# Kernel tuning notes

Hardware: AMD Instinct MI355X
Metric: run time of the kernel (lower is better)

The kernel has to match this reference:

```python
import jax, jax.numpy as jnp
import numpy as np

MAXG = 8          # max adaptive sampling grid (boxes generated so ceil(roi_size) <= 8)
SCALE = 0.125     # spatial_scale / ds (ds = 1.0)


def setup_inputs() -> dict:
    key = jax.random.key(0)
    ks = jax.random.split(key, 12)
    bs, N, ch, H, W = 8, 128, 1280, 64, 64
    out_ch, inner = 1024, 5120
    z = jax.random.normal(ks[0], (bs, ch, H, W), jnp.float32)
    # boxes (x1, y1, x2, y2) in 512x512 image coords, sizes in [8, 64] px
    x1 = jax.random.uniform(ks[1], (bs, N), minval=0.0, maxval=448.0)
    y1 = jax.random.uniform(ks[2], (bs, N), minval=0.0, maxval=448.0)
    bw = jax.random.uniform(ks[3], (bs, N), minval=8.0, maxval=64.0)
    bh = jax.random.uniform(ks[4], (bs, N), minval=8.0, maxval=64.0)
    bboxes = jnp.stack([x1, y1, x1 + bw, y1 + bh], axis=-1)

    def lin(k, fan_in, shape):
        return jax.random.normal(k, shape, jnp.float32) * (1.0 / np.sqrt(fan_in))

    W1 = lin(ks[5], ch, (ch, inner)); b1 = jnp.zeros((inner,), jnp.float32)
    W2 = lin(ks[6], inner, (inner, out_ch)); b2 = jnp.zeros((out_ch,), jnp.float32)
    S1 = lin(ks[7], 2, (2, 64)); sb1 = jnp.zeros((64,), jnp.float32)
    S2 = lin(ks[8], 64, (64, 256)); sb2 = jnp.zeros((256,), jnp.float32)
    S3 = lin(ks[9], 256, (256, out_ch)); sb3 = jnp.zeros((out_ch,), jnp.float32)
    O = lin(ks[10], 2 * out_ch, (2 * out_ch, out_ch)); ob = jnp.zeros((out_ch,), jnp.float32)
    return dict(z=z, bboxes=bboxes, W1=W1, b1=b1, W2=W2, b2=b2,
                S1=S1, sb1=sb1, S2=S2, sb2=sb2, S3=S3, sb3=sb3, O=O, ob=ob)


def _prep(c, size):
    # torchvision bilinear border handling for one coordinate axis
    oob = (c < -1.0) | (c > size)
    cc = jnp.clip(c, 0.0, None)
    lo0 = jnp.floor(cc)
    hi_case = lo0 >= size - 1
    lo = jnp.minimum(lo0, size - 1).astype(jnp.int32)
    hi = jnp.minimum(lo0 + 1, size - 1).astype(jnp.int32)
    frac = jnp.where(hi_case, 0.0, cc - lo0)
    return lo, hi, frac, oob


def _roi_align_1x1(z, bboxes):
    # torchvision roi_align, output_size=1, aligned=True, sampling_ratio=-1
    bs, ch, H, W = z.shape
    N = bboxes.shape[1]
    boxes = jax.lax.stop_gradient(bboxes).reshape(-1, 4) * SCALE - 0.5  # aligned
    bidx = jnp.repeat(jnp.arange(bs), N)
    rw = boxes[:, 2] - boxes[:, 0]
    rh = boxes[:, 3] - boxes[:, 1]
    gw = jnp.clip(jnp.ceil(rw), 1, MAXG)   # adaptive grid: ceil(roi_size / 1)
    gh = jnp.clip(jnp.ceil(rh), 1, MAXG)
    count = gh * gw
    i = jnp.arange(MAXG, dtype=jnp.float32)
    ys = boxes[:, 1:2] + (i[None] + 0.5) * rh[:, None] / gh[:, None]  # [R, G]
    xs = boxes[:, 0:1] + (i[None] + 0.5) * rw[:, None] / gw[:, None]
    vy = i[None] < gh[:, None]
    vx = i[None] < gw[:, None]
    yl, yh, fy, oy = _prep(ys, H)
    xl, xh, fx, ox = _prep(xs, W)
    my = (vy & ~oy).astype(z.dtype)
    mx = (vx & ~ox).astype(z.dtype)
    mask = my[:, :, None] * mx[:, None, :]             # [R, G, G]
    hy, ly = 1.0 - fy, fy
    hx, lx = 1.0 - fx, fx
    zt = jnp.transpose(z, (0, 2, 3, 1))                # [bs, H, W, ch]
    acc = jnp.zeros((bs * N, ch), z.dtype)
    corners = [(yl, xl, hy, hx), (yl, xh, hy, lx), (yh, xl, ly, hx), (yh, xh, ly, lx)]
    for yi, xi, wy, wx in corners:
        wt = mask * (wy[:, :, None] * wx[:, None, :])  # [R, G, G]
        v = zt[bidx[:, None, None], yi[:, :, None], xi[:, None, :]]  # [R, G, G, ch]
        acc = acc + jnp.einsum('rgh,rghc->rc', wt, v)
    return (acc / count[:, None]).reshape(bs, N, ch)


def reference(z, bboxes, W1, b1, W2, b2, S1, sb1, S2, sb2, S3, sb3, O, ob):
    x = _roi_align_1x1(z, bboxes)                      # [bs, N, ch]
    x = jax.nn.relu(x @ W1 + b1) @ W2 + b2             # out MLP
    # BBoxSizeEmbedder: (h, w) = (y2 - y1, x2 - x1)
    sz = jnp.stack([bboxes[..., 3] - bboxes[..., 1],
                    bboxes[..., 2] - bboxes[..., 0]], axis=-1)
    e = jax.nn.relu(sz @ S1 + sb1)
    e = jax.nn.relu(e @ S2 + sb2)
    e = e @ S3 + sb3
    return jnp.concatenate([x, e], axis=-1) @ O + ob   # out2
```

## Files before the change

kernel.cpp:

```cpp
#include <hip/hip_runtime.h>

static constexpr int kBS    = 8;
static constexpr int kNROI  = 128;
static constexpr int kR     = kBS * kNROI;
static constexpr int kCH    = 1280;
static constexpr int kH     = 64;
static constexpr int kW     = 64;
static constexpr int kPIX   = kH * kW;
static constexpr int kINNER = 5120;
static constexpr int kOUTC  = 1024;
static constexpr int kXE    = 2 * kOUTC;
static constexpr int kE2    = 256;
static constexpr int kLB    = 144;

typedef _Float16 half8 __attribute__((ext_vector_type(8)));
typedef float floatx4 __attribute__((ext_vector_type(4)));

__device__ __forceinline__ void gload_lds16(const _Float16* g, _Float16* l) {
    __builtin_amdgcn_global_load_lds(
        (const __attribute__((address_space(1))) void*)g,
        (__attribute__((address_space(3))) void*)l,
        16, 0, 0);
}

static constexpr int kPrepListEnd = 4;
static constexpr int kPrepMlpEnd  = 260;
static constexpr int kPrepAllEnd  = 260 + 13824;

__global__ __launch_bounds__(256) void prep_all(const float* __restrict__ W1,
                                                const float* __restrict__ W2,
                                                const float* __restrict__ O,
                                                const float* __restrict__ S3,
                                                _Float16* __restrict__ W1t,
                                                _Float16* __restrict__ W2t,
                                                _Float16* __restrict__ Ot,
                                                _Float16* __restrict__ S3t,
                                                const float* __restrict__ bboxes,
                                                const float* __restrict__ S1,
                                                const float* __restrict__ sb1,
                                                const float* __restrict__ S2,
                                                const float* __restrict__ sb2,
                                                _Float16* __restrict__ h2f,
                                                int2* __restrict__ lst,
                                                int* __restrict__ npA) {
    __shared__ float smem[12 * 256 * 2];
    const int bid = blockIdx.x;
    const int t   = threadIdx.x;

    if (bid < kPrepListEnd) {
        float* yw = smem;
        float* xw = smem + 12 * 256;
        const int r = bid * 256 + t;
#pragma unroll
        for (int i = 0; i < 12; ++i) { yw[i * 256 + t] = 0.0f; xw[i * 256 + t] = 0.0f; }

        const float x1 = bboxes[r * 4 + 0] * 0.125f - 0.5f;
        const float y1 = bboxes[r * 4 + 1] * 0.125f - 0.5f;
        const float x2 = bboxes[r * 4 + 2] * 0.125f - 0.5f;
        const float y2 = bboxes[r * 4 + 3] * 0.125f - 0.5f;
        const float rw = x2 - x1, rh = y2 - y1;
        const float gwf = fminf(fmaxf(ceilf(rw), 1.0f), 8.0f);
        const float ghf = fminf(fmaxf(ceilf(rh), 1.0f), 8.0f);
        const int gw = (int)gwf, gh = (int)ghf;
        const float ic = 1.0f / (gwf * ghf);

        int ymin = 0, last = 0;
        for (int g = 0; g < gh; ++g) {
            const float c   = y1 + ((float)g + 0.5f) * rh / ghf;
            const bool oob  = (c < -1.0f) || (c > 64.0f);
            const float cc  = fmaxf(c, 0.0f);
            const float lo0 = floorf(cc);
            const bool hic  = (lo0 >= 63.0f);
            const int lo    = (int)fminf(lo0, 63.0f);
            const int hi    = (int)fminf(lo0 + 1.0f, 63.0f);
            const float fr  = hic ? 0.0f : (cc - lo0);
            const float m   = oob ? 0.0f : 1.0f;
            if (g == 0) ymin = lo;
            const int il = min(lo - ymin, 11);
            const int ih = min(hi - ymin, 11);
            yw[il * 256 + t] += m * (1.0f - fr);
            yw[ih * 256 + t] += m * fr;
            last = hi;
        }
        const int nyd = min(last - ymin + 1, 12);

        int xmin = 0; last = 0;
        for (int g = 0; g < gw; ++g) {
            const float c   = x1 + ((float)g + 0.5f) * rw / gwf;
            const bool oob  = (c < -1.0f) || (c > 64.0f);
            const float cc  = fmaxf(c, 0.0f);
            const float lo0 = floorf(cc);
            const bool hic  = (lo0 >= 63.0f);
            const int lo    = (int)fminf(lo0, 63.0f);
            const int hi    = (int)fminf(lo0 + 1.0f, 63.0f);
            const float fr  = hic ? 0.0f : (cc - lo0);
            const float m   = oob ? 0.0f : 1.0f;
            if (g == 0) xmin = lo;
            const int il = min(lo - xmin, 11);
            const int ih = min(hi - xmin, 11);
            xw[il * 256 + t] += m * (1.0f - fr);
            xw[ih * 256 + t] += m * fr;
            last = hi;
        }
        const int nxd = min(last - xmin + 1, 12);

        int2* lr = lst + (size_t)r * kLB;
        int p = 0;
        for (int iy = 0; iy < nyd; ++iy) {
            const float wy = yw[iy * 256 + t] * ic;
            const int yb   = (ymin + iy) * kW + xmin;
            for (int ix = 0; ix < nxd; ++ix) {
                const float w = wy * xw[ix * 256 + t];
                if (w != 0.0f) {
                    int2 e; e.x = yb + ix; e.y = __float_as_int(w);
                    lr[p++] = e;
                }
            }
        }
        npA[r] = p;
    } else if (bid < kPrepMlpEnd) {
        const int r0 = (bid - kPrepListEnd) * 4;
        float* sz = smem;
        float* h1 = smem + 8;
        if (t < 8) {
            const int row = t >> 1;
            const int c   = t & 1;
            const float* bb = bboxes + (size_t)(r0 + row) * 4;
            sz[row * 2 + c] = (c == 0) ? (bb[3] - bb[1]) : (bb[2] - bb[0]);
        }
        __syncthreads();
        {
            const int row = t >> 6;
            const int j   = t & 63;
            const float v = sz[row * 2] * S1[j] + sz[row * 2 + 1] * S1[64 + j] + sb1[j];
            h1[row * 64 + j] = fmaxf(v, 0.0f);
        }
        __syncthreads();
        {
            float acc[4];
            const float b = sb2[t];
#pragma unroll
            for (int row = 0; row < 4; ++row) acc[row] = b;
#pragma unroll 16
            for (int k = 0; k < 64; ++k) {
                const float w = S2[k * 256 + t];
#pragma unroll
                for (int row = 0; row < 4; ++row) acc[row] += h1[row * 64 + k] * w;
            }
#pragma unroll
            for (int row = 0; row < 4; ++row)
                h2f[(size_t)(r0 + row) * kE2 + t] = (_Float16)fmaxf(acc[row], 0.0f);
        }
    } else {
        const int cb = bid - kPrepMlpEnd;
        const float* W; _Float16* Wt; int K, N, tile;
        if (cb < 6400)        { W = W1; Wt = W1t; K = kCH;    N = kINNER; tile = cb; }
        else if (cb < 11520)  { W = W2; Wt = W2t; K = kINNER; N = kOUTC;  tile = cb - 6400; }
        else if (cb < 13568)  { W = O;  Wt = Ot;  K = kXE;    N = kOUTC;  tile = cb - 11520; }
        else                  { W = S3; Wt = S3t; K = kE2;    N = kOUTC;  tile = cb - 13568; }
        const int nt = N / 32;
        const int n0 = (tile % nt) * 32;
        const int k0 = (tile / nt) * 32;
        {
            const int row = t >> 3;
            const int c4  = (t & 7) * 4;
            const float4 v = *(const float4*)&W[(size_t)(k0 + row) * N + n0 + c4];
            float* tl = smem + row * 33 + c4;
            tl[0] = v.x; tl[1] = v.y; tl[2] = v.z; tl[3] = v.w;
        }
        __syncthreads();
        {
            const int n  = t >> 3;
            const int k4 = (t & 7) * 4;
            union { _Float16 h[4]; uint2 u; } pk;
#pragma unroll
            for (int j = 0; j < 4; ++j) pk.h[j] = (_Float16)smem[(k4 + j) * 33 + n];
            *(uint2*)&Wt[(size_t)(n0 + n) * K + k0 + k4] = pk.u;
        }
    }
}

static constexpr int kPC = 4;
static constexpr int kPS = 4112;

__global__ __launch_bounds__(256) void roi_gather_planes(const float* __restrict__ z,
                                                         const int2* __restrict__ lst,
                                                         const int* __restrict__ npA,
                                                         _Float16* __restrict__ x) {
    __shared__ float pl[kPC * kPS];
    const int chg = blockIdx.x;
    const int b   = blockIdx.y;
    const int c0  = chg * kPC;
    const int t   = threadIdx.x;
    const float* zb = z + ((size_t)b * kCH + c0) * kPIX;
#pragma unroll
    for (int i = 0; i < 16; ++i) {
        const int idx = t + i * 256;
        const int ch  = idx >> 10;
        const int w4  = (idx & 1023) * 4;
        const float4 v = *(const float4*)&zb[(size_t)ch * kPIX + w4];
        *(float4*)&pl[ch * kPS + w4] = v;
    }
    __syncthreads();
    const int ch   = t & 3;
    const int slot = t >> 2;
    const float* plc = pl + ch * kPS;
#pragma unroll
    for (int rr = 0; rr < 2; ++rr) {
        const int r = b * kNROI + slot + rr * 64;
        const int np = npA[r];
        const int2* lr = lst + (size_t)r * kLB;
        float acc = 0.0f;
        for (int p = 0; p < np; ++p) {
            const int2 e = lr[p];
            acc += __int_as_float(e.y) * plc[e.x];
        }
        x[(size_t)r * kCH + c0 + ch] = (_Float16)acc;
    }
}

template <int NSPLIT>
__global__ __launch_bounds__(256) void gemm_f16_sk(const _Float16* __restrict__ A,
                                                   const _Float16* __restrict__ Bt,
                                                   float* __restrict__ P,
                                                   int Kfull) {
    __shared__ _Float16 As[2][128 * 32];
    __shared__ _Float16 Bs[2][128 * 32];
    const int t    = threadIdx.x;
    const int lane = t & 63;
    const int wave = t >> 6;
    const int m0 = blockIdx.y * 128, n0 = blockIdx.x * 128;
    const int Ksplit = Kfull / NSPLIT;
    const int s  = blockIdx.z;
    const int Nn = gridDim.x * 128;
    const int Mm = gridDim.y * 128;

    const int c0 = t, c1 = t + 256;
    const _Float16* Ag0 = A + (size_t)(m0 + (c0 >> 2)) * Kfull + (c0 & 3) * 8 + s * Ksplit;
    const _Float16* Ag1 = A + (size_t)(m0 + (c1 >> 2)) * Kfull + (c1 & 3) * 8 + s * Ksplit;
    const _Float16* Bg0 = Bt + (size_t)(n0 + (c0 >> 2)) * Kfull + (c0 & 3) * 8 + s * Ksplit;
    const _Float16* Bg1 = Bt + (size_t)(n0 + (c1 >> 2)) * Kfull + (c1 & 3) * 8 + s * Ksplit;

    const int wm = (wave >> 1) * 64;
    const int wn = (wave & 1) * 64;
    const int fm = lane & 15;
    const int kq = (lane >> 4) * 8;

    floatx4 acc[4][4];
#pragma unroll
    for (int i = 0; i < 4; ++i)
#pragma unroll
        for (int j = 0; j < 4; ++j) acc[i][j] = (floatx4){0.f, 0.f, 0.f, 0.f};

    const int nsteps = Ksplit / 32;
    gload_lds16(Ag0, &As[0][c0 * 8]);
    gload_lds16(Ag1, &As[0][c1 * 8]);
    gload_lds16(Bg0, &Bs[0][c0 * 8]);
    gload_lds16(Bg1, &Bs[0][c1 * 8]);
    __syncthreads();

    for (int ks = 0; ks < nsteps; ++ks) {
        const int cur = ks & 1;
        if (ks + 1 < nsteps) {
            const int kn = (ks + 1) * 32;
            gload_lds16(Ag0 + kn, &As[cur ^ 1][c0 * 8]);
            gload_lds16(Ag1 + kn, &As[cur ^ 1][c1 * 8]);
            gload_lds16(Bg0 + kn, &Bs[cur ^ 1][c0 * 8]);
            gload_lds16(Bg1 + kn, &Bs[cur ^ 1][c1 * 8]);
        }
        half8 af[4], bfv[4];
#pragma unroll
        for (int i = 0; i < 4; ++i)
            af[i] = *(const half8*)&As[cur][(wm + i * 16 + fm) * 32 + kq];
#pragma unroll
        for (int j = 0; j < 4; ++j)
            bfv[j] = *(const half8*)&Bs[cur][(wn + j * 16 + fm) * 32 + kq];
#pragma unroll
        for (int i = 0; i < 4; ++i)
#pragma unroll
            for (int j = 0; j < 4; ++j)
                acc[i][j] = __builtin_amdgcn_mfma_f32_16x16x32_f16(af[i], bfv[j], acc[i][j], 0, 0, 0);
        __syncthreads();
    }

    float* Pp = P + (size_t)s * Mm * Nn;
    const int qr = (lane >> 4) * 4;
#pragma unroll
    for (int j = 0; j < 4; ++j) {
        const int col = n0 + wn + j * 16 + fm;
#pragma unroll
        for (int i = 0; i < 4; ++i) {
            const int row = m0 + wm + i * 16 + qr;
#pragma unroll
            for (int rr = 0; rr < 4; ++rr)
                Pp[(size_t)(row + rr) * Nn + col] = acc[i][j][rr];
        }
    }
}

__global__ __launch_bounds__(256) void gemm_dual(const _Float16* __restrict__ h2f,
                                                 const _Float16* __restrict__ S3t,
                                                 const float* __restrict__ sb3,
                                                 _Float16* __restrict__ xeR,
                                                 const _Float16* __restrict__ x,
                                                 const _Float16* __restrict__ W1t,
                                                 const float* __restrict__ b1,
                                                 _Float16* __restrict__ h) {
    __shared__ _Float16 As[2][128 * 32];
    __shared__ _Float16 Bs[2][128 * 32];
    const int bid = blockIdx.x;
    const _Float16* A; const _Float16* Bt; const float* bias; _Float16* Out;
    int Kfull, ldc, nbn, tile; bool relu;
    if (bid < 64) {
        A = h2f; Bt = S3t; bias = sb3; Out = xeR;
        Kfull = kE2; ldc = kXE; relu = false; nbn = kOUTC / 128; tile = bid;
    } else {
        A = x; Bt = W1t; bias = b1; Out = h;
        Kfull = kCH; ldc = kINNER; relu = true; nbn = kINNER / 128; tile = bid - 64;
    }
    const int n0 = (tile % nbn) * 128;
    const int m0 = (tile / nbn) * 128;

    const int t    = threadIdx.x;
    const int lane = t & 63;
    const int wave = t >> 6;

    const int c0 = t, c1 = t + 256;
    const _Float16* Ag0 = A + (size_t)(m0 + (c0 >> 2)) * Kfull + (c0 & 3) * 8;
    const _Float16* Ag1 = A + (size_t)(m0 + (c1 >> 2)) * Kfull + (c1 & 3) * 8;
    const _Float16* Bg0 = Bt + (size_t)(n0 + (c0 >> 2)) * Kfull + (c0 & 3) * 8;
    const _Float16* Bg1 = Bt + (size_t)(n0 + (c1 >> 2)) * Kfull + (c1 & 3) * 8;

    const int wm = (wave >> 1) * 64;
    const int wn = (wave & 1) * 64;
    const int fm = lane & 15;
    const int kq = (lane >> 4) * 8;

    floatx4 acc[4][4];
#pragma unroll
    for (int i = 0; i < 4; ++i)
#pragma unroll
        for (int j = 0; j < 4; ++j) acc[i][j] = (floatx4){0.f, 0.f, 0.f, 0.f};

    const int nsteps = Kfull / 32;
    gload_lds16(Ag0, &As[0][c0 * 8]);
    gload_lds16(Ag1, &As[0][c1 * 8]);
    gload_lds16(Bg0, &Bs[0][c0 * 8]);
    gload_lds16(Bg1, &Bs[0][c1 * 8]);
    __syncthreads();

    for (int ks = 0; ks < nsteps; ++ks) {
        const int cur = ks & 1;
        if (ks + 1 < nsteps) {
            const int kn = (ks + 1) * 32;
            gload_lds16(Ag0 + kn, &As[cur ^ 1][c0 * 8]);
            gload_lds16(Ag1 + kn, &As[cur ^ 1][c1 * 8]);
            gload_lds16(Bg0 + kn, &Bs[cur ^ 1][c0 * 8]);
            gload_lds16(Bg1 + kn, &Bs[cur ^ 1][c1 * 8]);
        }
        half8 af[4], bfv[4];
#pragma unroll
        for (int i = 0; i < 4; ++i)
            af[i] = *(const half8*)&As[cur][(wm + i * 16 + fm) * 32 + kq];
#pragma unroll
        for (int j = 0; j < 4; ++j)
            bfv[j] = *(const half8*)&Bs[cur][(wn + j * 16 + fm) * 32 + kq];
#pragma unroll
        for (int i = 0; i < 4; ++i)
#pragma unroll
            for (int j = 0; j < 4; ++j)
                acc[i][j] = __builtin_amdgcn_mfma_f32_16x16x32_f16(af[i], bfv[j], acc[i][j], 0, 0, 0);
        __syncthreads();
    }

    const int qr = (lane >> 4) * 4;
#pragma unroll
    for (int j = 0; j < 4; ++j) {
        const int col = n0 + wn + j * 16 + fm;
        const float bv = bias[col];
#pragma unroll
        for (int i = 0; i < 4; ++i) {
            const int row = m0 + wm + i * 16 + qr;
#pragma unroll
            for (int rr = 0; rr < 4; ++rr) {
                float v = acc[i][j][rr] + bv;
                if (relu) v = fmaxf(v, 0.f);
                Out[(size_t)(row + rr) * ldc + col] = (_Float16)v;
            }
        }
    }
}

template <bool RELU, bool F16OUT, int NSPLIT>
__global__ __launch_bounds__(256) void reduce_splitk(const float* __restrict__ P,
                                                     const float* __restrict__ bias,
                                                     void* __restrict__ Cout,
                                                     int Nn, int ldc) {
    const size_t idx = ((size_t)blockIdx.x * 256 + threadIdx.x) * 4;
    const size_t MN  = (size_t)gridDim.x * 1024;
    const int m = (int)(idx / (size_t)Nn);
    const int n = (int)(idx % (size_t)Nn);
    float4 acc = *(const float4*)(P + idx);
#pragma unroll
    for (int s = 1; s < NSPLIT; ++s) {
        const float4 v = *(const float4*)(P + (size_t)s * MN + idx);
        acc.x += v.x; acc.y += v.y; acc.z += v.z; acc.w += v.w;
    }
    const float4 b4 = *(const float4*)(bias + n);
    acc.x += b4.x; acc.y += b4.y; acc.z += b4.z; acc.w += b4.w;
    if (RELU) {
        acc.x = fmaxf(acc.x, 0.f); acc.y = fmaxf(acc.y, 0.f);
        acc.z = fmaxf(acc.z, 0.f); acc.w = fmaxf(acc.w, 0.f);
    }
    if (F16OUT) {
        union { _Float16 h[4]; uint2 u; } pk;
        pk.h[0] = (_Float16)acc.x; pk.h[1] = (_Float16)acc.y;
        pk.h[2] = (_Float16)acc.z; pk.h[3] = (_Float16)acc.w;
        *(uint2*)((_Float16*)Cout + (size_t)m * ldc + n) = pk.u;
    } else {
        *(float4*)((float*)Cout + (size_t)m * ldc + n) = acc;
    }
}

extern "C" void kernel_launch(void* const* d_in, const int* in_sizes, int n_in,
                              void* d_out, int out_size, void* d_ws, size_t ws_size,
                              hipStream_t stream) {
    (void)in_sizes; (void)n_in; (void)out_size; (void)ws_size;
    const float* z   = (const float*)d_in[0];
    const float* bb  = (const float*)d_in[1];
    const float* W1  = (const float*)d_in[2];
    const float* b1  = (const float*)d_in[3];
    const float* W2  = (const float*)d_in[4];
    const float* b2  = (const float*)d_in[5];
    const float* S1  = (const float*)d_in[6];
    const float* sb1 = (const float*)d_in[7];
    const float* S2  = (const float*)d_in[8];
    const float* sb2 = (const float*)d_in[9];
    const float* S3  = (const float*)d_in[10];
    const float* sb3 = (const float*)d_in[11];
    const float* O   = (const float*)d_in[12];
    const float* ob  = (const float*)d_in[13];
    float* out = (float*)d_out;

    char* ws = (char*)d_ws;
    size_t off = 0;
    auto alloc = [&](size_t bytes) {
        void* p = ws + off;
        off += (bytes + 255) & ~(size_t)255;
        return p;
    };
    _Float16* x    = (_Float16*)alloc((size_t)kR * kCH * 2);
    _Float16* h    = (_Float16*)alloc((size_t)kR * kINNER * 2);
    _Float16* xe   = (_Float16*)alloc((size_t)kR * kXE * 2);
    _Float16* W1t  = (_Float16*)alloc((size_t)kINNER * kCH * 2);
    _Float16* W2t  = (_Float16*)alloc((size_t)kOUTC * kINNER * 2);
    _Float16* Ot   = (_Float16*)alloc((size_t)kOUTC * kXE * 2);
    _Float16* S3t  = (_Float16*)alloc((size_t)kOUTC * kE2 * 2);
    _Float16* h2f  = (_Float16*)alloc((size_t)kR * kE2 * 2);
    int2*     lst  = (int2*)alloc((size_t)kR * kLB * 8);
    int*      npA  = (int*)alloc((size_t)kR * 4);
    float*    P    = (float*)alloc((size_t)8 * kR * kOUTC * 4);

    hipLaunchKernelGGL(prep_all, dim3(kPrepAllEnd), dim3(256), 0, stream,
                       W1, W2, O, S3, W1t, W2t, Ot, S3t,
                       bb, S1, sb1, S2, sb2, h2f, lst, npA);

    hipLaunchKernelGGL(roi_gather_planes, dim3(kCH / kPC, kBS), dim3(256), 0, stream,
                       z, lst, npA, x);

    hipLaunchKernelGGL(gemm_dual, dim3(64 + (kINNER / 128) * (kR / 128)), dim3(256), 0,
                       stream, h2f, S3t, sb3, xe + kOUTC, x, W1t, b1, h);

    hipLaunchKernelGGL((gemm_f16_sk<8>), dim3(kOUTC / 128, kR / 128, 8), dim3(256), 0,
                       stream, h, W2t, P, kINNER);
    hipLaunchKernelGGL((reduce_splitk<false, true, 8>),
                       dim3((size_t)kR * kOUTC / 1024), dim3(256), 0, stream,
                       P, b2, xe, kOUTC, kXE);

    hipLaunchKernelGGL((gemm_f16_sk<8>), dim3(kOUTC / 128, kR / 128, 8), dim3(256), 0,
                       stream, xe, Ot, P, kXE);
    hipLaunchKernelGGL((reduce_splitk<false, false, 8>),
                       dim3((size_t)kR * kOUTC / 1024), dim3(256), 0, stream,
                       P, ob, out, kOUTC, kOUTC);
}
```

Baseline: 406.9 us.

## Fuse ROI gather into prep kernel, recompute separable bilinear weights per block

Merges the ROI-align gather into the front prep kernel so it runs concurrently with the weight transpose and size MLP, removing one launch and the serial dependency between the list build and the gather. Each gather block now recomputes the separable y/x bilinear weights for its 128 ROIs in shared memory instead of reading a precomputed sparse (index, weight) list from global memory. Channels per block drop from 4 to 2, so there are more gather blocks. The cost is redundant per-block weight computation (only half the threads work during it), and a larger shared-memory footprint for the weight-transpose and MLP blocks that share this kernel, which may lower their occupancy.

```diff
diff --git a/kernel.cpp b/kernel.cpp
--- a/kernel.cpp
+++ b/kernel.cpp
@@ -11,7 +11,6 @@
 static constexpr int kOUTC  = 1024;
 static constexpr int kXE    = 2 * kOUTC;
 static constexpr int kE2    = 256;
-static constexpr int kLB    = 144;
 
 typedef _Float16 half8 __attribute__((ext_vector_type(8)));
 typedef float floatx4 __attribute__((ext_vector_type(4)));
@@ -23,103 +22,123 @@
         16, 0, 0);
 }
 
-static constexpr int kPrepListEnd = 4;
-static constexpr int kPrepMlpEnd  = 260;
-static constexpr int kPrepAllEnd  = 260 + 13824;
-
-__global__ __launch_bounds__(256) void prep_all(const float* __restrict__ W1,
-                                                const float* __restrict__ W2,
-                                                const float* __restrict__ O,
-                                                const float* __restrict__ S3,
-                                                _Float16* __restrict__ W1t,
-                                                _Float16* __restrict__ W2t,
-                                                _Float16* __restrict__ Ot,
-                                                _Float16* __restrict__ S3t,
-                                                const float* __restrict__ bboxes,
-                                                const float* __restrict__ S1,
-                                                const float* __restrict__ sb1,
-                                                const float* __restrict__ S2,
-                                                const float* __restrict__ sb2,
-                                                _Float16* __restrict__ h2f,
-                                                int2* __restrict__ lst,
-                                                int* __restrict__ npA) {
-    __shared__ float smem[12 * 256 * 2];
+static constexpr int kPC = 2;
+static constexpr int kPS = 4100;
+static constexpr int kFGat = (kCH / kPC) * kBS;
+static constexpr int kFMlp = kFGat + 256;
+static constexpr int kFAll = kFMlp + 13824;
+
+__global__ __launch_bounds__(256) void front_all(const float* __restrict__ z,
+                                                 const float* __restrict__ bboxes,
+                                                 const float* __restrict__ W1,
+                                                 const float* __restrict__ W2,
+                                                 const float* __restrict__ O,
+                                                 const float* __restrict__ S3,
+                                                 _Float16* __restrict__ W1t,
+                                                 _Float16* __restrict__ W2t,
+                                                 _Float16* __restrict__ Ot,
+                                                 _Float16* __restrict__ S3t,
+                                                 const float* __restrict__ S1,
+                                                 const float* __restrict__ sb1,
+                                                 const float* __restrict__ S2,
+                                                 const float* __restrict__ sb2,
+                                                 _Float16* __restrict__ h2f,
+                                                 _Float16* __restrict__ x) {
+    __shared__ float smem[kPC * kPS + 12 * 128 + 12 * 128 + 512];
     const int bid = blockIdx.x;
     const int t   = threadIdx.x;
 
-    if (bid < kPrepListEnd) {
-        float* yw = smem;
-        float* xw = smem + 12 * 256;
-        const int r = bid * 256 + t;
-#pragma unroll
-        for (int i = 0; i < 12; ++i) { yw[i * 256 + t] = 0.0f; xw[i * 256 + t] = 0.0f; }
-
-        const float x1 = bboxes[r * 4 + 0] * 0.125f - 0.5f;
-        const float y1 = bboxes[r * 4 + 1] * 0.125f - 0.5f;
-        const float x2 = bboxes[r * 4 + 2] * 0.125f - 0.5f;
-        const float y2 = bboxes[r * 4 + 3] * 0.125f - 0.5f;
-        const float rw = x2 - x1, rh = y2 - y1;
-        const float gwf = fminf(fmaxf(ceilf(rw), 1.0f), 8.0f);
-        const float ghf = fminf(fmaxf(ceilf(rh), 1.0f), 8.0f);
-        const int gw = (int)gwf, gh = (int)ghf;
-        const float ic = 1.0f / (gwf * ghf);
-
-        int ymin = 0, last = 0;
-        for (int g = 0; g < gh; ++g) {
-            const float c   = y1 + ((float)g + 0.5f) * rh / ghf;
-            const bool oob  = (c < -1.0f) || (c > 64.0f);
-            const float cc  = fmaxf(c, 0.0f);
-            const float lo0 = floorf(cc);
-            const bool hic  = (lo0 >= 63.0f);
-            const int lo    = (int)fminf(lo0, 63.0f);
-            const int hi    = (int)fminf(lo0 + 1.0f, 63.0f);
-            const float fr  = hic ? 0.0f : (cc - lo0);
-            const float m   = oob ? 0.0f : 1.0f;
-            if (g == 0) ymin = lo;
-            const int il = min(lo - ymin, 11);
-            const int ih = min(hi - ymin, 11);
-            yw[il * 256 + t] += m * (1.0f - fr);
-            yw[ih * 256 + t] += m * fr;
-            last = hi;
-        }
-        const int nyd = min(last - ymin + 1, 12);
-
-        int xmin = 0; last = 0;
-        for (int g = 0; g < gw; ++g) {
-            const float c   = x1 + ((float)g + 0.5f) * rw / gwf;
-            const bool oob  = (c < -1.0f) || (c > 64.0f);
-            const float cc  = fmaxf(c, 0.0f);
-            const float lo0 = floorf(cc);
-            const bool hic  = (lo0 >= 63.0f);
-            const int lo    = (int)fminf(lo0, 63.0f);
-            const int hi    = (int)fminf(lo0 + 1.0f, 63.0f);
-            const float fr  = hic ? 0.0f : (cc - lo0);
-            const float m   = oob ? 0.0f : 1.0f;
-            if (g == 0) xmin = lo;
-            const int il = min(lo - xmin, 11);
-            const int ih = min(hi - xmin, 11);
-            xw[il * 256 + t] += m * (1.0f - fr);
-            xw[ih * 256 + t] += m * fr;
-            last = hi;
-        }
-        const int nxd = min(last - xmin + 1, 12);
-
-        int2* lr = lst + (size_t)r * kLB;
-        int p = 0;
-        for (int iy = 0; iy < nyd; ++iy) {
-            const float wy = yw[iy * 256 + t] * ic;
-            const int yb   = (ymin + iy) * kW + xmin;
-            for (int ix = 0; ix < nxd; ++ix) {
-                const float w = wy * xw[ix * 256 + t];
-                if (w != 0.0f) {
-                    int2 e; e.x = yb + ix; e.y = __float_as_int(w);
-                    lr[p++] = e;
-                }
+    if (bid < kFGat) {
+        float* pl  = smem;
+        float* ywL = smem + kPC * kPS;
+        float* xwL = ywL + 12 * 128;
+        int*   im  = (int*)(xwL + 12 * 128);
+        const int b   = bid & 7;
+        const int chg = bid >> 3;
+        const int c0  = chg * kPC;
+        const float* zb = z + ((size_t)b * kCH + c0) * kPIX;
+#pragma unroll
+        for (int i = 0; i < 8; ++i) {
+            const int idx = t + i * 256;
+            const int ch  = idx >> 10;
+            const int w4  = (idx & 1023) * 4;
+            const float4 v = *(const float4*)&zb[(size_t)ch * kPIX + w4];
+            *(float4*)&pl[ch * kPS + w4] = v;
+        }
+        if (t < 128) {
+            const int r = b * kNROI + t;
+#pragma unroll
+            for (int i = 0; i < 12; ++i) { ywL[i * 128 + t] = 0.0f; xwL[i * 128 + t] = 0.0f; }
+            const float x1 = bboxes[r * 4 + 0] * 0.125f - 0.5f;
+            const float y1 = bboxes[r * 4 + 1] * 0.125f - 0.5f;
+            const float x2 = bboxes[r * 4 + 2] * 0.125f - 0.5f;
+            const float y2 = bboxes[r * 4 + 3] * 0.125f - 0.5f;
+            const float rw = x2 - x1, rh = y2 - y1;
+            const float gwf = fminf(fmaxf(ceilf(rw), 1.0f), 8.0f);
+            const float ghf = fminf(fmaxf(ceilf(rh), 1.0f), 8.0f);
+            const int gw = (int)gwf, gh = (int)ghf;
+            const float ic = 1.0f / (gwf * ghf);
+
+            int ymin = 0, last = 0;
+            for (int g = 0; g < gh; ++g) {
+                const float c   = y1 + ((float)g + 0.5f) * rh / ghf;
+                const bool oob  = (c < -1.0f) || (c > 64.0f);
+                const float cc  = fmaxf(c, 0.0f);
+                const float lo0 = floorf(cc);
+                const bool hic  = (lo0 >= 63.0f);
+                const int lo    = (int)fminf(lo0, 63.0f);
+                const int hi    = (int)fminf(lo0 + 1.0f, 63.0f);
+                const float fr  = hic ? 0.0f : (cc - lo0);
+                const float m   = oob ? 0.0f : 1.0f;
+                if (g == 0) ymin = lo;
+                const int il = min(lo - ymin, 11);
+                const int ih = min(hi - ymin, 11);
+                ywL[il * 128 + t] += m * (1.0f - fr);
+                ywL[ih * 128 + t] += m * fr;
+                last = hi;
             }
-        }
-        npA[r] = p;
-    } else if (bid < kPrepMlpEnd) {
-        const int r0 = (bid - kPrepListEnd) * 4;
+            const int nyd = min(last - ymin + 1, 12);
+
+            int xmin = 0; last = 0;
+            for (int g = 0; g < gw; ++g) {
+                const float c   = x1 + ((float)g + 0.5f) * rw / gwf;
+                const bool oob  = (c < -1.0f) || (c > 64.0f);
+                const float cc  = fmaxf(c, 0.0f);
+                const float lo0 = floorf(cc);
+                const bool hic  = (lo0 >= 63.0f);
+                const int lo    = (int)fminf(lo0, 63.0f);
+                const int hi    = (int)fminf(lo0 + 1.0f, 63.0f);
+                const float fr  = hic ? 0.0f : (cc - lo0);
+                const float m   = oob ? 0.0f : 1.0f;
+                if (g == 0) xmin = lo;
+                const int il = min(lo - xmin, 11);
+                const int ih = min(hi - xmin, 11);
+                xwL[il * 128 + t] += m * (1.0f - fr);
+                xwL[ih * 128 + t] += m * fr;
+                last = hi;
+            }
+            const int nxd = min(last - xmin + 1, 12);
+#pragma unroll
+            for (int i = 0; i < 12; ++i) ywL[i * 128 + t] *= ic;
+            im[t] = ymin; im[128 + t] = xmin; im[256 + t] = nyd; im[384 + t] = nxd;
+        }
+        __syncthreads();
+        const int ch = t & 1;
+        const int ri = t >> 1;
+        const int r  = b * kNROI + ri;
+        const float* plc = pl + ch * kPS;
+        const int ym = im[ri], xm = im[128 + ri];
+        const int ny = im[256 + ri], nx = im[384 + ri];
+        float acc = 0.0f;
+        for (int iy = 0; iy < ny; ++iy) {
+            const float wy = ywL[iy * 128 + ri];
+            const int ro   = (ym + iy) * kW + xm;
+            for (int ix = 0; ix < nx; ++ix)
+                acc += wy * xwL[ix * 128 + ri] * plc[ro + ix];
+        }
+        x[(size_t)r * kCH + c0 + ch] = (_Float16)acc;
+    } else if (bid < kFMlp) {
+        const int r0 = (bid - kFGat) * 4;
         float* sz = smem;
         float* h1 = smem + 8;
         if (t < 8) {
@@ -152,7 +171,7 @@
                 h2f[(size_t)(r0 + row) * kE2 + t] = (_Float16)fmaxf(acc[row], 0.0f);
         }
     } else {
-        const int cb = bid - kPrepMlpEnd;
+        const int cb = bid - kFMlp;
         const float* W; _Float16* Wt; int K, N, tile;
         if (cb < 6400)        { W = W1; Wt = W1t; K = kCH;    N = kINNER; tile = cb; }
         else if (cb < 11520)  { W = W2; Wt = W2t; K = kINNER; N = kOUTC;  tile = cb - 6400; }
@@ -177,45 +196,6 @@
             for (int j = 0; j < 4; ++j) pk.h[j] = (_Float16)smem[(k4 + j) * 33 + n];
             *(uint2*)&Wt[(size_t)(n0 + n) * K + k0 + k4] = pk.u;
         }
-    }
-}
-
-static constexpr int kPC = 4;
-static constexpr int kPS = 4112;
-
-__global__ __launch_bounds__(256) void roi_gather_planes(const float* __restrict__ z,
-                                                         const int2* __restrict__ lst,
-                                                         const int* __restrict__ npA,
-                                                         _Float16* __restrict__ x) {
-    __shared__ float pl[kPC * kPS];
-    const int chg = blockIdx.x;
-    const int b   = blockIdx.y;
-    const int c0  = chg * kPC;
-    const int t   = threadIdx.x;
-    const float* zb = z + ((size_t)b * kCH + c0) * kPIX;
-#pragma unroll
-    for (int i = 0; i < 16; ++i) {
-        const int idx = t + i * 256;
-        const int ch  = idx >> 10;
-        const int w4  = (idx & 1023) * 4;
-        const float4 v = *(const float4*)&zb[(size_t)ch * kPIX + w4];
-        *(float4*)&pl[ch * kPS + w4] = v;
-    }
-    __syncthreads();
-    const int ch   = t & 3;
-    const int slot = t >> 2;
-    const float* plc = pl + ch * kPS;
-#pragma unroll
-    for (int rr = 0; rr < 2; ++rr) {
-        const int r = b * kNROI + slot + rr * 64;
-        const int np = npA[r];
-        const int2* lr = lst + (size_t)r * kLB;
-        float acc = 0.0f;
-        for (int p = 0; p < np; ++p) {
-            const int2 e = lr[p];
-            acc += __int_as_float(e.y) * plc[e.x];
-        }
-        x[(size_t)r * kCH + c0 + ch] = (_Float16)acc;
     }
 }
 
@@ -457,16 +437,11 @@
     _Float16* Ot   = (_Float16*)alloc((size_t)kOUTC * kXE * 2);
     _Float16* S3t  = (_Float16*)alloc((size_t)kOUTC * kE2 * 2);
     _Float16* h2f  = (_Float16*)alloc((size_t)kR * kE2 * 2);
-    int2*     lst  = (int2*)alloc((size_t)kR * kLB * 8);
-    int*      npA  = (int*)alloc((size_t)kR * 4);
     float*    P    = (float*)alloc((size_t)8 * kR * kOUTC * 4);
 
-    hipLaunchKernelGGL(prep_all, dim3(kPrepAllEnd), dim3(256), 0, stream,
-                       W1, W2, O, S3, W1t, W2t, Ot, S3t,
-                       bb, S1, sb1, S2, sb2, h2f, lst, npA);
-
-    hipLaunchKernelGGL(roi_gather_planes, dim3(kCH / kPC, kBS), dim3(256), 0, stream,
-                       z, lst, npA, x);
+    hipLaunchKernelGGL(front_all, dim3(kFAll), dim3(256), 0, stream,
+                       z, bb, W1, W2, O, S3, W1t, W2t, Ot, S3t,
+                       S1, sb1, S2, sb2, h2f, x);
 
     hipLaunchKernelGGL(gemm_dual, dim3(64 + (kINNER / 128) * (kR / 128)), dim3(256), 0,
                        stream, h2f, S3t, sb3, xe + kOUTC, x, W1t, b1, h);
```

Measured after the change: 398.0 us. 1.02x faster.
